# Kernel optimization log

Measured on AMD Instinct MI355X. Metric: run time of the kernel, lower is better.

Reference implementation:

```python
import math
import jax, jax.numpy as jnp
from jax import lax
import numpy as np

N = 32768
IN_C = 64
OUT_C = 128
RATIO = 0.25
K = 16
BN_EPS = 1e-5


def setup_inputs() -> dict:
    key = jax.random.key(0)
    k1, k2, k3 = jax.random.split(key, 3)
    x = jax.random.normal(k1, (N, IN_C), dtype=jnp.float32)
    pos = jax.random.normal(k2, (N, 3), dtype=jnp.float32)
    batch = jnp.zeros((N,), dtype=jnp.int32)  # single point cloud
    # MLP params: Linear(IN_C, OUT_C) + BatchNorm1d(OUT_C)
    W = jax.random.normal(k3, (IN_C, OUT_C), dtype=jnp.float32) / np.sqrt(IN_C)
    b = jnp.zeros((OUT_C,), dtype=jnp.float32)
    gamma = jnp.ones((OUT_C,), dtype=jnp.float32)
    beta = jnp.zeros((OUT_C,), dtype=jnp.float32)
    return {"x": x, "pos": pos, "batch": batch, "W": W, "b": b, "gamma": gamma, "beta": beta}


def _fps(pos, m):
    """Farthest point sampling: returns m indices. Deterministic start at index 0."""
    d0 = jnp.sum((pos - pos[0]) ** 2, axis=-1)  # [N]

    def step(min_d, _):
        idx = jnp.argmax(min_d)
        d = jnp.sum((pos - pos[idx]) ** 2, axis=-1)
        return jnp.minimum(min_d, d), idx

    _, rest = lax.scan(step, d0, None, length=m - 1)
    return jnp.concatenate([jnp.zeros((1,), dtype=rest.dtype), rest])


def _knn(pos, query, k):
    """For each query point, indices of its k nearest points in pos. [M,k]"""
    # squared distances [M, N] via (q-p)^2 = |q|^2 - 2 q.p + |p|^2
    d2 = (jnp.sum(query * query, axis=-1, keepdims=True)
          - 2.0 * (query @ pos.T)
          + jnp.sum(pos * pos, axis=-1)[None, :])
    _, nn_idx = lax.top_k(-d2, k)
    return nn_idx


def reference(x, pos, batch, W, b, gamma, beta):
    m = int(math.ceil(RATIO * pos.shape[0]))
    id_clusters = _fps(pos, m)                 # [M]
    sub_pos = pos[id_clusters]                 # [M, 3]
    sub_batch = batch[id_clusters]             # [M]
    nn_idx = _knn(pos, sub_pos, K)             # [M, K]

    # MLP: Linear -> BatchNorm1d (training-mode batch stats) -> ReLU
    h = x @ W + b                              # [N, OUT_C]
    mean = jnp.mean(h, axis=0)
    var = jnp.mean((h - mean) ** 2, axis=0)    # biased var, as BN uses
    h = (h - mean) * lax.rsqrt(var + BN_EPS) * gamma + beta
    feat = jax.nn.relu(h)

    # scatter_max over exactly-K neighbors per cluster == max over gathered [M,K,C]
    out = jnp.max(feat[nn_idx], axis=1)        # [M, OUT_C]
    return out, sub_pos, sub_batch
```

## Files before the change

kernel.cpp:

```cpp
#include <hip/hip_runtime.h>
#include <float.h>

#define N_PTS 32768
#define M_CL  8192
#define IN_C  64
#define OUT_C 128
#define K_NN  16
constexpr float BN_EPS_C = 1e-5f;


__global__ void zero_kernel(int* __restrict__ hist, int* __restrict__ cur) {
    int i = blockIdx.x * 256 + threadIdx.x;
    if (i < 4096) { hist[i] = 0; cur[i] = 0; }
}

__device__ __forceinline__ unsigned sp4(unsigned x) {
    x = (x | (x << 4)) & 0xC3u;
    x = (x | (x << 2)) & 0x249u;
    return x;
}

__global__ void prep_kernel(const float* __restrict__ pos,
                            float* __restrict__ px, float* __restrict__ py, float* __restrict__ pz,
                            int* __restrict__ cellid, int* __restrict__ hist) {
    int i = blockIdx.x * 256 + threadIdx.x;
    if (i >= N_PTS) return;
    float x = pos[3 * i + 0], y = pos[3 * i + 1], z = pos[3 * i + 2];
    px[i] = x; py[i] = y; pz[i] = z;
    int cx = (int)floorf((x + 4.0f) * 2.0f); cx = min(15, max(0, cx));
    int cy = (int)floorf((y + 4.0f) * 2.0f); cy = min(15, max(0, cy));
    int cz = (int)floorf((z + 4.0f) * 2.0f); cz = min(15, max(0, cz));
    int c = (int)(sp4((unsigned)cx) | (sp4((unsigned)cy) << 1) | (sp4((unsigned)cz) << 2));
    cellid[i] = c;
    atomicAdd(&hist[c], 1);
}

__global__ __launch_bounds__(1024) void scan_kernel(const int* __restrict__ hist,
                                                    int* __restrict__ start) {
    __shared__ int wtotI[16];
    const int tid = threadIdx.x;
    const int lane = tid & 63, w = tid >> 6;
    int4 hv = *reinterpret_cast<const int4*>(&hist[tid * 4]);
    int a0 = hv.x, a1 = a0 + hv.y, a2 = a1 + hv.z, a3 = a2 + hv.w;
    int tsum = a3;
    int v = tsum;
    #pragma unroll
    for (int off = 1; off < 64; off <<= 1) {
        int o = __shfl_up(v, off);
        if (lane >= off) v += o;
    }
    if (lane == 63) wtotI[w] = v;
    __syncthreads();
    if (tid < 16) {
        int v2 = wtotI[tid];
        #pragma unroll
        for (int off = 1; off < 16; off <<= 1) {
            int o = __shfl_up(v2, off);
            if (tid >= off) v2 += o;
        }
        wtotI[tid] = v2;
    }
    __syncthreads();
    int base = (w > 0 ? wtotI[w - 1] : 0) + (v - tsum);
    int4 sv;
    sv.x = base; sv.y = base + a0; sv.z = base + a1; sv.w = base + a2;
    *reinterpret_cast<int4*>(&start[tid * 4]) = sv;
}

__global__ void scatter_kernel(const float* __restrict__ px, const float* __restrict__ py,
                               const float* __restrict__ pz, const int* __restrict__ cellid,
                               const int* __restrict__ start, int* __restrict__ cur,
                               float4* __restrict__ pts4) {
    int i = blockIdx.x * 256 + threadIdx.x;
    if (i >= N_PTS) return;
    int c = cellid[i];
    int p = start[c] + atomicAdd(&cur[c], 1);
    pts4[p] = make_float4(px[i], py[i], pz[i], __uint_as_float((unsigned)i));
}

__device__ __forceinline__ unsigned long long shfl_xor_u64(unsigned long long v, int off) {
    unsigned lo = (unsigned)v, hi = (unsigned)(v >> 32);
    lo = __shfl_xor(lo, off);
    hi = __shfl_xor(hi, off);
    return ((unsigned long long)hi << 32) | (unsigned long long)lo;
}

__device__ __forceinline__ void region_update(
    int rr, float4 cc, float mm, float sx, float sy, float sz, int lane,
    float* __restrict__ mdL, unsigned long long* __restrict__ ckeyL,
    float4* __restrict__ cc4L, int* __restrict__ dirty) {
    #pragma clang fp contract(off)
    float dx = cc.x - sx;
    float dy = cc.y - sy;
    float dz = cc.z - sz;
    float xx = dx * dx, yy = dy * dy, zz = dz * dz;
    float d = (xx + yy) + zz;
    float nm = fminf(mm, d);
    bool chg = nm < mm;
    if (chg) mdL[(rr << 6) + lane] = nm;
    if (__ballot(chg)) {
        unsigned long long rk = ckeyL[rr];
        float cmaxR = __uint_as_float((unsigned)(rk >> 32));
        unsigned idxR = 0x7fffffffu - (unsigned)(rk & 0xffffffffu);
        unsigned oo = __float_as_uint(cc.w);
        bool danger = chg && ((oo == idxR) || (nm == cmaxR));
        if (__ballot(danger)) {
            unsigned long long kp = ((unsigned long long)__float_as_uint(nm) << 32)
                                  | (unsigned long long)(0x7fffffffu - oo);
            unsigned long long wp = kp;
            #pragma unroll
            for (int off = 32; off; off >>= 1) {
                unsigned long long ok = shfl_xor_u64(wp, off);
                if (ok > wp) wp = ok;
            }
            if (kp == wp) {
                ckeyL[rr] = wp;
                cc4L[rr] = make_float4(cc.x, cc.y, cc.z, 0.0f);
                dirty[rr >> 6] = 1;
            }
        }
    }
}

__global__ __launch_bounds__(512) void fps_kernel(
    const float4* __restrict__ pts4, const float* __restrict__ pos,
    int* __restrict__ ids, float* __restrict__ out_subpos) {
    #pragma clang fp contract(off)
    __shared__ __align__(16) float mdL[N_PTS];
    __shared__ __align__(16) float4 cen4L[512];
    __shared__ __align__(16) float4 cc4L[512];
    __shared__ unsigned long long ckeyL[512];
    __shared__ unsigned long long partK[8];
    __shared__ __align__(16) float4 partC[8];
    __shared__ int queue[512];
    __shared__ int qcnt;
    __shared__ int dirty[8];

    const int tid = threadIdx.x;
    const int lane = tid & 63, w = tid >> 6;

    const float s0x = pos[0], s0y = pos[1], s0z = pos[2];

    for (int k = 0; k < 64; ++k) {
        const int r = (w << 6) + k;
        const int gi = (r << 6) + lane;
        float4 c = pts4[gi];
        float X = c.x, Y = c.y, Z = c.z;
        unsigned o = __float_as_uint(c.w);
        float mnx = X, mxx = X, mny = Y, mxy = Y, mnz = Z, mxz = Z;
        float dx = X - s0x;
        float dy = Y - s0y;
        float dz = Z - s0z;
        float xx = dx * dx, yy = dy * dy, zz = dz * dz;
        float d = (xx + yy) + zz;
        mdL[gi] = d;
        unsigned long long kp = ((unsigned long long)__float_as_uint(d) << 32)
                              | (unsigned long long)(0x7fffffffu - o);
        unsigned long long wp = kp;
        #pragma unroll
        for (int off = 32; off; off >>= 1) {
            unsigned long long ok = shfl_xor_u64(wp, off);
            if (ok > wp) wp = ok;
            mnx = fminf(mnx, __shfl_xor(mnx, off)); mxx = fmaxf(mxx, __shfl_xor(mxx, off));
            mny = fminf(mny, __shfl_xor(mny, off)); mxy = fmaxf(mxy, __shfl_xor(mxy, off));
            mnz = fminf(mnz, __shfl_xor(mnz, off)); mxz = fmaxf(mxz, __shfl_xor(mxz, off));
        }
        if (kp == wp) {
            cc4L[r] = make_float4(X, Y, Z, 0.0f);
            ckeyL[r] = wp;
        }
        float cx = 0.5f * (mnx + mxx), cy = 0.5f * (mny + mxy), cz = 0.5f * (mnz + mxz);
        float rx = X - cx, ry = Y - cy, rz = Z - cz;
        float r2 = (rx * rx + ry * ry) + rz * rz;
        #pragma unroll
        for (int off = 32; off; off >>= 1) r2 = fmaxf(r2, __shfl_xor(r2, off));
        if (lane == 0) {
            float rd = sqrtf(r2) * 1.0005f + 1e-6f;
            cen4L[r] = make_float4(cx, cy, cz, rd);
        }
    }
    if (tid == 0) {
        ids[0] = 0;
        out_subpos[0] = s0x; out_subpos[1] = s0y; out_subpos[2] = s0z;
        qcnt = 0;
    }
    if (tid < 8) dirty[tid] = 0;
    __syncthreads();
    {
        const int rr = (w << 6) + lane;
        unsigned long long myk = ckeyL[rr];
        unsigned long long wk = myk;
        #pragma unroll
        for (int off = 32; off; off >>= 1) {
            unsigned long long ok = shfl_xor_u64(wk, off);
            if (ok > wk) wk = ok;
        }
        if (myk == wk) {
            partK[w] = wk;
            float4 wc = cc4L[rr];
            partC[w] = make_float4(wc.x, wc.y, wc.z, 0.0f);
        }
    }
    __syncthreads();

    for (int t = 1; t < M_CL; ++t) {
        unsigned long long myk = partK[lane & 7];
        unsigned long long bk = myk;
        #pragma unroll
        for (int off = 4; off; off >>= 1) {
            unsigned long long ok = shfl_xor_u64(bk, off);
            if (ok > bk) bk = ok;
        }
        unsigned long long eqm = __ballot(myk == bk);
        int slot = ((int)__ffsll(eqm) - 1) & 7;
        float4 s4 = partC[slot];
        const float sx = s4.x, sy = s4.y, sz = s4.z;
        if (tid == 0) {
            ids[t] = (int)(0x7fffffffu - (unsigned)(bk & 0xffffffffu));
            out_subpos[3 * t + 0] = sx;
            out_subpos[3 * t + 1] = sy;
            out_subpos[3 * t + 2] = sz;
        }
        float4 cr = cen4L[tid];
        float ex = sx - cr.x, ey = sy - cr.y, ez = sz - cr.z;
        float dc2 = (ex * ex + ey * ey) + ez * ez;
        float lb = sqrtf(dc2) * 0.9995f - cr.w;
        float cmaxf = __uint_as_float((unsigned)(ckeyL[tid] >> 32));
        bool aff = !(lb > 0.0f && lb * lb * 0.999f >= cmaxf);
        unsigned long long mB = __ballot(aff);
        {
            int cnt = __popcll(mB);
            int base = 0;
            if (lane == 0 && cnt) base = atomicAdd(&qcnt, cnt);
            base = __shfl(base, 0);
            if (aff) queue[base + (int)__popcll(mB & ((1ull << lane) - 1ull))] = tid;
        }
        __syncthreads();

        const int qn = qcnt;
        if (w < qn) {
            int r0 = -1, r1 = -1, r2 = -1;
            float4 c0, c1, c2; float m0 = 0, m1 = 0, m2 = 0;
            c0 = c1 = c2 = make_float4(0, 0, 0, 0);
            {
                r0 = queue[w];
                c0 = pts4[(r0 << 6) + lane];
                m0 = mdL[(r0 << 6) + lane];
            }
            if (w + 8 < qn) {
                r1 = queue[w + 8];
                c1 = pts4[(r1 << 6) + lane];
                m1 = mdL[(r1 << 6) + lane];
            }
            if (w + 16 < qn) {
                r2 = queue[w + 16];
                c2 = pts4[(r2 << 6) + lane];
                m2 = mdL[(r2 << 6) + lane];
            }
            for (int i = w; i < qn; i += 8) {
                region_update(r0, c0, m0, sx, sy, sz, lane, mdL, ckeyL, cc4L, dirty);
                r0 = r1; c0 = c1; m0 = m1;
                r1 = r2; c1 = c2; m1 = m2;
                const int iN = i + 24;
                if (iN < qn) {
                    r2 = queue[iN];
                    c2 = pts4[(r2 << 6) + lane];
                    m2 = mdL[(r2 << 6) + lane];
                } else {
                    r2 = -1;
                }
            }
        }
        __syncthreads();

        if (tid == 0) qcnt = 0;
        if (dirty[w]) {
            const int rr = (w << 6) + lane;
            unsigned long long myk2 = ckeyL[rr];
            unsigned long long wk = myk2;
            #pragma unroll
            for (int off = 32; off; off >>= 1) {
                unsigned long long ok = shfl_xor_u64(wk, off);
                if (ok > wk) wk = ok;
            }
            if (myk2 == wk) {
                partK[w] = wk;
                float4 wc = cc4L[rr];
                partC[w] = make_float4(wc.x, wc.y, wc.z, 0.0f);
                dirty[w] = 0;
            }
        }
        __syncthreads();
    }
}

__global__ void sub_batch_kernel(const int* __restrict__ ids, const int* __restrict__ batch,
                                 float* __restrict__ sub_batch) {
    int i = blockIdx.x * 256 + threadIdx.x;
    if (i < M_CL) sub_batch[i] = (float)batch[ids[i]];
}

__global__ __launch_bounds__(256) void gemm_stats_kernel(
    const float* __restrict__ x, const float* __restrict__ W, const float* __restrict__ bias,
    float* __restrict__ h, float* __restrict__ psum, float* __restrict__ psumsq) {
    __shared__ __align__(16) float Wl[64 * 128];
    __shared__ float xl[64 * 64];
    __shared__ float st[8 * 128 * 2];

    const int t = threadIdx.x;
    const int r0 = blockIdx.x * 64;
    #pragma unroll
    for (int u = 0; u < 32; ++u) Wl[u * 256 + t] = W[u * 256 + t];
    #pragma unroll
    for (int u = 0; u < 16; ++u) { int f = u * 256 + t; xl[f] = x[r0 * 64 + f]; }
    __syncthreads();

    const int cg = t & 31;
    const int rg = t >> 5;
    float acc[8][4];
    #pragma unroll
    for (int j = 0; j < 8; ++j)
        #pragma unroll
        for (int cc = 0; cc < 4; ++cc) acc[j][cc] = 0.0f;

    #pragma unroll 4
    for (int k = 0; k < 64; ++k) {
        float4 w4 = *reinterpret_cast<const float4*>(&Wl[k * 128 + cg * 4]);
        #pragma unroll
        for (int j = 0; j < 8; ++j) {
            float xv = xl[(rg * 8 + j) * 64 + k];
            acc[j][0] = fmaf(xv, w4.x, acc[j][0]);
            acc[j][1] = fmaf(xv, w4.y, acc[j][1]);
            acc[j][2] = fmaf(xv, w4.z, acc[j][2]);
            acc[j][3] = fmaf(xv, w4.w, acc[j][3]);
        }
    }
    float4 b4 = *reinterpret_cast<const float4*>(&bias[cg * 4]);
    float s1[4] = {0, 0, 0, 0}, s2[4] = {0, 0, 0, 0};
    #pragma unroll
    for (int j = 0; j < 8; ++j) {
        float4 hv;
        hv.x = acc[j][0] + b4.x;
        hv.y = acc[j][1] + b4.y;
        hv.z = acc[j][2] + b4.z;
        hv.w = acc[j][3] + b4.w;
        *reinterpret_cast<float4*>(&h[(r0 + rg * 8 + j) * 128 + cg * 4]) = hv;
        s1[0] += hv.x; s2[0] += hv.x * hv.x;
        s1[1] += hv.y; s2[1] += hv.y * hv.y;
        s1[2] += hv.z; s2[2] += hv.z * hv.z;
        s1[3] += hv.w; s2[3] += hv.w * hv.w;
    }
    #pragma unroll
    for (int cc = 0; cc < 4; ++cc) {
        st[(rg * 128 + cg * 4 + cc) * 2 + 0] = s1[cc];
        st[(rg * 128 + cg * 4 + cc) * 2 + 1] = s2[cc];
    }
    __syncthreads();
    if (t < 128) {
        float a = 0.0f, q = 0.0f;
        #pragma unroll
        for (int g = 0; g < 8; ++g) {
            a += st[(g * 128 + t) * 2 + 0];
            q += st[(g * 128 + t) * 2 + 1];
        }
        psum[blockIdx.x * 128 + t] = a;
        psumsq[blockIdx.x * 128 + t] = q;
    }
}

__global__ void bn_finalize_kernel(const float* __restrict__ psum, const float* __restrict__ psumsq,
                                   const float* __restrict__ gamma, const float* __restrict__ beta,
                                   float* __restrict__ scale, float* __restrict__ shift) {
    int c = threadIdx.x;
    float s = 0.0f, q = 0.0f;
    #pragma unroll 8
    for (int p = 0; p < 512; ++p) {
        s += psum[p * 128 + c];
        q += psumsq[p * 128 + c];
    }
    float mean = s * (1.0f / N_PTS);
    float var = q * (1.0f / N_PTS) - mean * mean;
    float sc = gamma[c] * rsqrtf(var + BN_EPS_C);
    scale[c] = sc;
    shift[c] = beta[c] - mean * sc;
}

__global__ __launch_bounds__(256) void knn_kernel(
    const float* __restrict__ posx, const float* __restrict__ posy, const float* __restrict__ posz,
    const int* __restrict__ ids, int* __restrict__ nn) {
    const int lane = threadIdx.x & 63;
    const int q = blockIdx.x * 4 + (threadIdx.x >> 6);
    const int qi = ids[q];
    const float qx = posx[qi], qy = posy[qi], qz = posz[qi];

    float dv[16]; int di[16];
    #pragma unroll
    for (int j = 0; j < 16; ++j) { dv[j] = FLT_MAX; di[j] = 0x7fffffff; }
    float wm = FLT_MAX; int wmi = 0x7fffffff; int wslot = 0;

    for (int s = 0; s < N_PTS / 64; ++s) {
        int i = s * 64 + lane;
        float dx = posx[i] - qx, dy = posy[i] - qy, dz = posz[i] - qz;
        float d = fmaf(dx, dx, fmaf(dy, dy, dz * dz));
        if (d < wm || (d == wm && i < wmi)) {
            #pragma unroll
            for (int j = 0; j < 16; ++j)
                if (j == wslot) { dv[j] = d; di[j] = i; }
            wm = -1.0f; wmi = -1;
            #pragma unroll
            for (int j = 0; j < 16; ++j) {
                bool g = (dv[j] > wm) || (dv[j] == wm && di[j] > wmi);
                if (g) { wm = dv[j]; wmi = di[j]; wslot = j; }
            }
        }
    }
    for (int rr = 0; rr < 16; ++rr) {
        float bv = FLT_MAX; int bidx = 0x7fffffff;
        #pragma unroll
        for (int j = 0; j < 16; ++j) {
            bool g = (dv[j] < bv) || (dv[j] == bv && di[j] < bidx);
            if (g) { bv = dv[j]; bidx = di[j]; }
        }
        #pragma unroll
        for (int off = 32; off; off >>= 1) {
            float ov = __shfl_xor(bv, off);
            int oi = __shfl_xor(bidx, off);
            if (ov < bv || (ov == bv && oi < bidx)) { bv = ov; bidx = oi; }
        }
        if (lane == 0) nn[q * 16 + rr] = bidx;
        #pragma unroll
        for (int j = 0; j < 16; ++j)
            if (di[j] == bidx) { dv[j] = FLT_MAX; di[j] = 0x7fffffff; }
    }
}

__global__ __launch_bounds__(256) void pool_kernel(
    const float* __restrict__ h, const int* __restrict__ nn,
    const float* __restrict__ scale, const float* __restrict__ shift,
    float* __restrict__ out) {
    const int t = threadIdx.x;
    const int c = t & 127;
    const int m = blockIdx.x * 2 + (t >> 7);
    const float sc = scale[c], sh = shift[c];
    float mx = -FLT_MAX;
    #pragma unroll
    for (int k = 0; k < 16; ++k) {
        int n = nn[m * 16 + k];
        float hv = h[n * 128 + c];
        mx = fmaxf(mx, fmaf(hv, sc, sh));
    }
    out[m * 128 + c] = fmaxf(mx, 0.0f);
}

extern "C" void kernel_launch(void* const* d_in, const int* in_sizes, int n_in,
                              void* d_out, int out_size, void* d_ws, size_t ws_size,
                              hipStream_t stream) {
    const float* x     = (const float*)d_in[0];
    const float* pos   = (const float*)d_in[1];
    const int*   batch = (const int*)d_in[2];
    const float* W     = (const float*)d_in[3];
    const float* b     = (const float*)d_in[4];
    const float* gamma = (const float*)d_in[5];
    const float* beta  = (const float*)d_in[6];
    (void)in_sizes; (void)n_in; (void)out_size; (void)ws_size;

    float* out       = (float*)d_out;
    float* sub_pos   = out + (size_t)M_CL * OUT_C;
    float* sub_batch = sub_pos + (size_t)M_CL * 3;

    char* w8 = (char*)d_ws;
    float*  posx   = (float*) (w8 + 0);
    float*  posy   = (float*) (w8 + 131072);
    float*  posz   = (float*) (w8 + 262144);
    float4* pts4   = (float4*)(w8 + 393216);
    int*    cellid = (int*)   (w8 + 917504);
    int*    hist   = (int*)   (w8 + 1048576);
    int*    startb = (int*)   (w8 + 1064960);
    int*    cur    = (int*)   (w8 + 1081344);
    int*    ids    = (int*)   (w8 + 1097728);
    int*    nn     = (int*)   (w8 + 1130496);
    float* psum   = (float*)(w8 + 393216);
    float* psumsq = (float*)(w8 + 655360);
    float* scale  = (float*)(w8 + 1048576);
    float* shift  = (float*)(w8 + 1049088);
    float* h      = (float*)(w8 + 2097152);

    zero_kernel<<<32, 256, 0, stream>>>(hist, cur);
    prep_kernel<<<128, 256, 0, stream>>>(pos, posx, posy, posz, cellid, hist);
    scan_kernel<<<1, 1024, 0, stream>>>(hist, startb);
    scatter_kernel<<<128, 256, 0, stream>>>(posx, posy, posz, cellid, startb, cur, pts4);
    fps_kernel<<<1, 512, 0, stream>>>(pts4, pos, ids, sub_pos);
    sub_batch_kernel<<<32, 256, 0, stream>>>(ids, batch, sub_batch);
    gemm_stats_kernel<<<512, 256, 0, stream>>>(x, W, b, h, psum, psumsq);
    bn_finalize_kernel<<<1, 128, 0, stream>>>(psum, psumsq, gamma, beta, scale, shift);
    knn_kernel<<<2048, 256, 0, stream>>>(posx, posy, posz, ids, nn);
    pool_kernel<<<4096, 256, 0, stream>>>(h, nn, scale, shift, out);
}
```

Baseline: 19.81 ms.

## Replace shared work queue with per-wave self-owned region processing in FPS

The FPS loop no longer compacts affected regions into a block-wide shared queue with an atomic counter and an extra barrier. Each wave now processes only the affected regions it owns, walking its ballot mask with a 3-deep prefetch, and tracks locally whether its argmax key changed. This removes one __syncthreads, the atomic, and the dirty flags from every iteration. The cost is possible load imbalance when affected regions cluster within a few waves, which leaves other waves idle.

```diff
diff --git a/kernel.cpp b/kernel.cpp
--- a/kernel.cpp
+++ b/kernel.cpp
@@ -85,10 +85,10 @@
     return ((unsigned long long)hi << 32) | (unsigned long long)lo;
 }
 
-__device__ __forceinline__ void region_update(
+__device__ __forceinline__ bool region_update(
     int rr, float4 cc, float mm, float sx, float sy, float sz, int lane,
     float* __restrict__ mdL, unsigned long long* __restrict__ ckeyL,
-    float4* __restrict__ cc4L, int* __restrict__ dirty) {
+    float4* __restrict__ cc4L) {
     #pragma clang fp contract(off)
     float dx = cc.x - sx;
     float dy = cc.y - sy;
@@ -116,10 +116,11 @@
             if (kp == wp) {
                 ckeyL[rr] = wp;
                 cc4L[rr] = make_float4(cc.x, cc.y, cc.z, 0.0f);
-                dirty[rr >> 6] = 1;
-            }
-        }
-    }
+            }
+            return true;
+        }
+    }
+    return false;
 }
 
 __global__ __launch_bounds__(512) void fps_kernel(
@@ -132,9 +133,6 @@
     __shared__ unsigned long long ckeyL[512];
     __shared__ unsigned long long partK[8];
     __shared__ __align__(16) float4 partC[8];
-    __shared__ int queue[512];
-    __shared__ int qcnt;
-    __shared__ int dirty[8];
 
     const int tid = threadIdx.x;
     const int lane = tid & 63, w = tid >> 6;
@@ -182,9 +180,7 @@
     if (tid == 0) {
         ids[0] = 0;
         out_subpos[0] = s0x; out_subpos[1] = s0y; out_subpos[2] = s0z;
-        qcnt = 0;
-    }
-    if (tid < 8) dirty[tid] = 0;
+    }
     __syncthreads();
     {
         const int rr = (w << 6) + lane;
@@ -221,60 +217,45 @@
             out_subpos[3 * t + 1] = sy;
             out_subpos[3 * t + 2] = sz;
         }
-        float4 cr = cen4L[tid];
+        const int myr = (w << 6) + lane;
+        float4 cr = cen4L[myr];
         float ex = sx - cr.x, ey = sy - cr.y, ez = sz - cr.z;
         float dc2 = (ex * ex + ey * ey) + ez * ez;
         float lb = sqrtf(dc2) * 0.9995f - cr.w;
-        float cmaxf = __uint_as_float((unsigned)(ckeyL[tid] >> 32));
+        float cmaxf = __uint_as_float((unsigned)(ckeyL[myr] >> 32));
         bool aff = !(lb > 0.0f && lb * lb * 0.999f >= cmaxf);
-        unsigned long long mB = __ballot(aff);
-        {
-            int cnt = __popcll(mB);
-            int base = 0;
-            if (lane == 0 && cnt) base = atomicAdd(&qcnt, cnt);
-            base = __shfl(base, 0);
-            if (aff) queue[base + (int)__popcll(mB & ((1ull << lane) - 1ull))] = tid;
-        }
-        __syncthreads();
-
-        const int qn = qcnt;
-        if (w < qn) {
+        unsigned long long m = __ballot(aff);
+
+        bool wchg = false;
+        if (m) {
+            unsigned long long mm = m;
             int r0 = -1, r1 = -1, r2 = -1;
             float4 c0, c1, c2; float m0 = 0, m1 = 0, m2 = 0;
             c0 = c1 = c2 = make_float4(0, 0, 0, 0);
-            {
-                r0 = queue[w];
-                c0 = pts4[(r0 << 6) + lane];
-                m0 = mdL[(r0 << 6) + lane];
-            }
-            if (w + 8 < qn) {
-                r1 = queue[w + 8];
-                c1 = pts4[(r1 << 6) + lane];
-                m1 = mdL[(r1 << 6) + lane];
-            }
-            if (w + 16 < qn) {
-                r2 = queue[w + 16];
-                c2 = pts4[(r2 << 6) + lane];
-                m2 = mdL[(r2 << 6) + lane];
-            }
-            for (int i = w; i < qn; i += 8) {
-                region_update(r0, c0, m0, sx, sy, sz, lane, mdL, ckeyL, cc4L, dirty);
+            r0 = (w << 6) + ((int)__ffsll(mm) - 1); mm &= mm - 1;
+            c0 = pts4[(r0 << 6) + lane]; m0 = mdL[(r0 << 6) + lane];
+            if (mm) {
+                r1 = (w << 6) + ((int)__ffsll(mm) - 1); mm &= mm - 1;
+                c1 = pts4[(r1 << 6) + lane]; m1 = mdL[(r1 << 6) + lane];
+            }
+            if (mm) {
+                r2 = (w << 6) + ((int)__ffsll(mm) - 1); mm &= mm - 1;
+                c2 = pts4[(r2 << 6) + lane]; m2 = mdL[(r2 << 6) + lane];
+            }
+            while (r0 >= 0) {
+                wchg |= region_update(r0, c0, m0, sx, sy, sz, lane, mdL, ckeyL, cc4L);
                 r0 = r1; c0 = c1; m0 = m1;
                 r1 = r2; c1 = c2; m1 = m2;
-                const int iN = i + 24;
-                if (iN < qn) {
-                    r2 = queue[iN];
-                    c2 = pts4[(r2 << 6) + lane];
-                    m2 = mdL[(r2 << 6) + lane];
+                if (mm) {
+                    r2 = (w << 6) + ((int)__ffsll(mm) - 1); mm &= mm - 1;
+                    c2 = pts4[(r2 << 6) + lane]; m2 = mdL[(r2 << 6) + lane];
                 } else {
                     r2 = -1;
                 }
             }
         }
-        __syncthreads();
-
-        if (tid == 0) qcnt = 0;
-        if (dirty[w]) {
+
+        if (wchg) {
             const int rr = (w << 6) + lane;
             unsigned long long myk2 = ckeyL[rr];
             unsigned long long wk = myk2;
@@ -287,7 +268,6 @@
                 partK[w] = wk;
                 float4 wc = cc4L[rr];
                 partC[w] = make_float4(wc.x, wc.y, wc.z, 0.0f);
-                dirty[w] = 0;
             }
         }
         __syncthreads();
```

Measured after the change: 40.53 ms. 105% more time.
